# Optimization experiments

Measured on AMD Instinct MI355X. Metric: run time of the kernel, lower is better.

The kernel has to match this reference:

```python
import jax, jax.numpy as jnp
import numpy as np

B, M = 32768, 200
NUM_LAYERS, OW, OH = 22, 11, 11
CNN_CH, HIDDEN = 128, 512
ACTION_NVEC = (9, 10)


def setup_inputs() -> dict:
    key = jax.random.key(0)
    ks = jax.random.split(key, 16)
    s = 0.02
    inp = {
        "observations": jax.random.randint(ks[0], (B, M, 3), 0, 256, dtype=jnp.int32),
        "max_vec": jnp.ones((NUM_LAYERS,), dtype=jnp.float32),
        "w_conv1": jax.random.normal(ks[1], (CNN_CH, NUM_LAYERS, 5, 5), jnp.float32) * s,
        "b_conv1": jnp.zeros((CNN_CH,), jnp.float32),
        "w_conv2": jax.random.normal(ks[2], (CNN_CH, CNN_CH, 3, 3), jnp.float32) * s,
        "b_conv2": jnp.zeros((CNN_CH,), jnp.float32),
        "w_fc": jax.random.normal(ks[3], (CNN_CH, HIDDEN // 2), jnp.float32) * s,
        "b_fc": jnp.zeros((HIDDEN // 2,), jnp.float32),
        "w_self": jax.random.normal(ks[4], (NUM_LAYERS, HIDDEN // 2), jnp.float32) * s,
        "b_self": jnp.zeros((HIDDEN // 2,), jnp.float32),
        "w_actor0": jax.random.normal(ks[5], (HIDDEN, ACTION_NVEC[0]), jnp.float32) * 0.01,
        "b_actor0": jnp.zeros((ACTION_NVEC[0],), jnp.float32),
        "w_actor1": jax.random.normal(ks[6], (HIDDEN, ACTION_NVEC[1]), jnp.float32) * 0.01,
        "b_actor1": jnp.zeros((ACTION_NVEC[1],), jnp.float32),
        "w_value": jax.random.normal(ks[7], (HIDDEN, 1), jnp.float32) * s,
        "b_value": jnp.zeros((1,), jnp.float32),
    }
    return inp


def _conv(x, w, b, stride):
    y = jax.lax.conv_general_dilated(
        x, w, window_strides=(stride, stride), padding="VALID",
        dimension_numbers=("NCHW", "OIHW", "NCHW"))
    return y + b[None, :, None, None]


def _encode(observations, max_vec, w_conv1, b_conv1, w_conv2, b_conv2,
            w_fc, b_fc, w_self, b_self):
    # torch: token_observations[token_observations == 255] = 0
    obs = jnp.where(observations == 255, 0, observations)
    coords = obs[..., 0]                       # [B, M]
    x_idx = (coords >> 4) & 15
    y_idx = coords & 15
    atr_idx = obs[..., 1]
    atr_val = obs[..., 2].astype(jnp.float32)
    # coords_byte != 255 is always True after the 255->0 rewrite above
    valid = (x_idx < OW) & (y_idx < OH) & (atr_idx < NUM_LAYERS)
    b_idx = jnp.broadcast_to(jnp.arange(obs.shape[0])[:, None], coords.shape)
    # route invalid tokens to a dummy batch slot B, then drop it
    b_idx = jnp.where(valid, b_idx, obs.shape[0])
    a_idx = jnp.where(valid, atr_idx, 0)
    xs = jnp.where(valid, x_idx, 0)
    ys = jnp.where(valid, y_idx, 0)
    box = jnp.zeros((obs.shape[0] + 1, NUM_LAYERS, OW, OH), jnp.float32)
    box = box.at[b_idx, a_idx, xs, ys].set(atr_val)[: obs.shape[0]]
    features = box / max_vec[None, :, None, None]
    self_feat = jax.nn.relu(features[:, :, 5, 5] @ w_self + b_self)   # [B, 256]
    h = jax.nn.relu(_conv(features, w_conv1, b_conv1, 3))             # [B,128,3,3]
    h = jax.nn.relu(_conv(h, w_conv2, b_conv2, 1))                    # [B,128,1,1]
    h = h.reshape(h.shape[0], -1)                                     # [B,128]
    cnn_feat = jax.nn.relu(h @ w_fc + b_fc)                           # [B,256]
    return jnp.concatenate([self_feat, cnn_feat], axis=1)             # [B,512]


def reference(observations, max_vec, w_conv1, b_conv1, w_conv2, b_conv2,
              w_fc, b_fc, w_self, b_self, w_actor0, b_actor0,
              w_actor1, b_actor1, w_value, b_value):
    hidden = _encode(observations, max_vec, w_conv1, b_conv1, w_conv2, b_conv2,
                     w_fc, b_fc, w_self, b_self)
    logits0 = hidden @ w_actor0 + b_actor0
    logits1 = hidden @ w_actor1 + b_actor1
    value = hidden @ w_value + b_value
    return (logits0, logits1, value, hidden)
```

## Files before the change

kernel.cpp:

```cpp
#include <hip/hip_runtime.h>
#include <hip/hip_bf16.h>

typedef unsigned int uint;
typedef unsigned short ushort;
typedef unsigned long long ull;
typedef __attribute__((ext_vector_type(8))) short short8;
typedef __attribute__((ext_vector_type(4))) float float4_;

#define B_TOT 32768
#define NL    22
#define HID0  ((long)B_TOT * 20)

#define W2F_OFF  0
#define WFCF_OFF 294912
#define WHF_OFF  360448
#define W1P_OFF  393216
#define H1_OFF   534272

__device__ __forceinline__ ushort f2bf(float v) {
  uint x = __float_as_uint(v);
  x += 0x7fffu + ((x >> 16) & 1u);
  return (ushort)(x >> 16);
}
__device__ __forceinline__ uint cvtpk(float lo, float hi) {
  uint r;
  asm volatile("v_cvt_pk_bf16_f32 %0, %1, %2" : "=v"(r) : "v"(lo), "v"(hi));
  return r;
}
struct u3 { uint x, y, z; };

extern "C" __global__ __launch_bounds__(256)
void k_prep(const float* __restrict__ wc1, const float* __restrict__ wc2,
            const float* __restrict__ wfc,
            const float* __restrict__ wa0, const float* __restrict__ wa1,
            const float* __restrict__ wv,
            ushort* __restrict__ w2f, ushort* __restrict__ wfcf,
            ushort* __restrict__ whf, uint* __restrict__ w1p)
{
  int i = blockIdx.x * 256 + threadIdx.x;
  if (i < 18432) {
    int l = i & 63, cg = (i >> 6) & 7, ks = i >> 9;
    int col = cg * 16 + (l & 15), kb = ks * 32 + (l >> 4) * 8;
    ushort t[8];
    #pragma unroll
    for (int j = 0; j < 8; ++j) t[j] = f2bf(wc2[col * 1152 + kb + j]);
    uint4 o = { (uint)t[0]|((uint)t[1]<<16), (uint)t[2]|((uint)t[3]<<16),
                (uint)t[4]|((uint)t[5]<<16), (uint)t[6]|((uint)t[7]<<16) };
    ((uint4*)w2f)[i] = o;
  } else if (i < 22528) {
    int i2 = i - 18432;
    int l = i2 & 63, cg = (i2 >> 6) & 15, ks = i2 >> 10;
    int col = cg * 16 + (l & 15), kb = ks * 32 + (l >> 4) * 8;
    ushort t[8];
    #pragma unroll
    for (int j = 0; j < 8; ++j) t[j] = f2bf(wfc[(kb + j) * 256 + col]);
    uint4 o = { (uint)t[0]|((uint)t[1]<<16), (uint)t[2]|((uint)t[3]<<16),
                (uint)t[4]|((uint)t[5]<<16), (uint)t[6]|((uint)t[7]<<16) };
    ((uint4*)wfcf)[i2] = o;
  } else if (i < 24576) {
    int i2 = i - 22528;
    int l = i2 & 63, cg = (i2 >> 6) & 1, ks = i2 >> 7;
    int col = cg * 16 + (l & 15), kb = ks * 32 + (l >> 4) * 8;
    ushort t[8];
    #pragma unroll
    for (int j = 0; j < 8; ++j) {
      int k = kb + j;
      float v = (col < 9)  ? wa0[k*9 + col]
              : (col < 19) ? wa1[k*10 + (col - 9)]
              : (col == 19) ? wv[k] : 0.f;
      t[j] = f2bf(v);
    }
    uint4 o = { (uint)t[0]|((uint)t[1]<<16), (uint)t[2]|((uint)t[3]<<16),
                (uint)t[4]|((uint)t[5]<<16), (uint)t[6]|((uint)t[7]<<16) };
    ((uint4*)whf)[i2] = o;
  } else if (i < 24576 + 35264) {
    int j = i - 24576;
    int l = j & 63, r = j >> 6;
    uint val = 0u;
    if (r < 550) {
      ushort lo_ = f2bf(wc1[(2*l)     * 550 + r]);
      ushort hi_ = f2bf(wc1[(2*l + 1) * 550 + r]);
      val = (uint)lo_ | ((uint)hi_ << 16);
    }
    w1p[j] = val;
  }
}

#define PROC_CONV(tk, acc0, acc1)                                          \
  {                                                                        \
    const int a = (int)((tk) >> 16), x = (int)(((tk) >> 12) & 15u),        \
              y = (int)(((tk) >> 8) & 15u);                                \
    const float rmv = __int_as_float(                                      \
        __builtin_amdgcn_readlane(__float_as_int(rm_own), a));             \
    const float fv = (float)((tk) & 255u) * rmv;                           \
    const int wbase = a * 25;                                              \
    _Pragma("unroll")                                                      \
    for (int ox = 0; ox < 3; ++ox) {                                       \
      int kx = x - 3 * ox;                                                 \
      if ((unsigned)kx > 4u) continue;              \
      _Pragma("unroll")                                                    \
      for (int oy = 0; oy < 3; ++oy) {                                     \
        int ky = y - 3 * oy;                                               \
        if ((unsigned)ky > 4u) continue;                                   \
        uint wu = w1p[(wbase + kx * 5 + ky) * 64 + lane];                  \
        acc0[ox*3+oy] = fmaf(fv, __uint_as_float(wu << 16),                \
                             acc0[ox*3+oy]);                               \
        acc1[ox*3+oy] = fmaf(fv, __uint_as_float(wu & 0xffff0000u),        \
                             acc1[ox*3+oy]);                               \
      }                                                                    \
    }                                                                      \
  }

extern "C" __global__ __launch_bounds__(256)
void k_encode(const int* __restrict__ obs, const float* __restrict__ maxvec,
              const uint* __restrict__ w1p, const float* __restrict__ bc1,
              const float* __restrict__ wself, const float* __restrict__ bself,
              float* __restrict__ out, ushort* __restrict__ h1g)
{
  __shared__ uint klist[8][64];

  const int tid = threadIdx.x, lane = tid & 63, w = tid >> 6;
  const long bA = (long)blockIdx.x * 8 + w * 2;
  const long bB = bA + 1;

  float rm_own = (lane < NL) ? (1.0f / maxvec[lane]) : 0.f;

  const uint* obA = (const uint*)obs + bA * 600;
  const uint* obB = (const uint*)obs + bB * 600;
  uint* klA = klist[w * 2 + 0];
  uint* klB = klist[w * 2 + 1];

  int cntA = 0, cntB = 0;
  #pragma unroll
  for (int r = 0; r < 4; ++r) {
    int m = r * 64 + lane;
    bool vA = false, vB = false; uint pkA = 0, pkB = 0;
    if (m < 200) {
      u3 tA = *(const u3*)(obA + m * 3);
      u3 tB = *(const u3*)(obB + m * 3);
      uint cA = tA.x, aA = tA.y, vvA = tA.z;
      uint cB = tB.x, aB = tB.y, vvB = tB.z;
      cA = (cA == 255u) ? 0u : cA;  aA = (aA == 255u) ? 0u : aA;  vvA = (vvA == 255u) ? 0u : vvA;
      cB = (cB == 255u) ? 0u : cB;  aB = (aB == 255u) ? 0u : aB;  vvB = (vvB == 255u) ? 0u : vvB;
      uint xA = (cA >> 4) & 15u, yA = cA & 15u;
      uint xB = (cB >> 4) & 15u, yB = cB & 15u;
      vA = (xA < 11u) && (yA < 11u) && (aA < NL);
      vB = (xB < 11u) && (yB < 11u) && (aB < NL);
      pkA = (aA << 16) | (xA << 12) | (yA << 8) | vvA;
      pkB = (aB << 16) | (xB << 12) | (yB << 8) | vvB;
    }
    ull balA = __ballot(vA);
    if (vA) {
      int pos = cntA + __popcll(balA & ((1ull << lane) - 1ull));
      if (pos < 64) klA[pos] = pkA;
    }
    cntA += __popcll(balA);
    ull balB = __ballot(vB);
    if (vB) {
      int pos = cntB + __popcll(balB & ((1ull << lane) - 1ull));
      if (pos < 64) klB[pos] = pkB;
    }
    cntB += __popcll(balB);
  }
  if (cntA > 64) cntA = 64;
  if (cntB > 64) cntB = 64;

  uint uA = (lane < cntA) ? klA[lane] : 0xffffffffu;
  uint uB = (lane < cntB) ? klB[lane] : 0xffffffffu;
  uint cellA = uA >> 8, cellB = uB >> 8;
  bool aliveA = (lane < cntA), aliveB = (lane < cntB);
  const int dmax = (cntA > cntB) ? cntA : cntB;
  for (int d = 1; d < dmax; ++d) {
    uint oA = __shfl_down(cellA, d);
    uint oB = __shfl_down(cellB, d);
    aliveA = aliveA && !((lane + d < cntA) && (oA == cellA));
    aliveB = aliveB && !((lane + d < cntB) && (oB == cellB));
  }
  const ull balA2 = __ballot(aliveA);
  const ull balB2 = __ballot(aliveB);

  float2 saA = {0.f,0.f}, sbA = {0.f,0.f}, saB = {0.f,0.f}, sbB = {0.f,0.f};
  {
    ull b55 = __ballot(aliveA && (((uA >> 12) & 15u) == 5u) && (((uA >> 8) & 15u) == 5u));
    while (b55) {
      int idx = __builtin_ctzll(b55); b55 &= b55 - 1ull;
      uint tk = (uint)__builtin_amdgcn_readlane((int)uA, idx);
      int a = tk >> 16;
      float rmv = __int_as_float(__builtin_amdgcn_readlane(__float_as_int(rm_own), a));
      float fv = (float)(tk & 255u) * rmv;
      const float2* ws2 = (const float2*)(wself + a * 256);
      float2 w0 = ws2[lane], w1 = ws2[64 + lane];
      saA.x = fmaf(fv, w0.x, saA.x);  saA.y = fmaf(fv, w0.y, saA.y);
      sbA.x = fmaf(fv, w1.x, sbA.x);  sbA.y = fmaf(fv, w1.y, sbA.y);
    }
    b55 = __ballot(aliveB && (((uB >> 12) & 15u) == 5u) && (((uB >> 8) & 15u) == 5u));
    while (b55) {
      int idx = __builtin_ctzll(b55); b55 &= b55 - 1ull;
      uint tk = (uint)__builtin_amdgcn_readlane((int)uB, idx);
      int a = tk >> 16;
      float rmv = __int_as_float(__builtin_amdgcn_readlane(__float_as_int(rm_own), a));
      float fv = (float)(tk & 255u) * rmv;
      const float2* ws2 = (const float2*)(wself + a * 256);
      float2 w0 = ws2[lane], w1 = ws2[64 + lane];
      saB.x = fmaf(fv, w0.x, saB.x);  saB.y = fmaf(fv, w0.y, saB.y);
      sbB.x = fmaf(fv, w1.x, sbB.x);  sbB.y = fmaf(fv, w1.y, sbB.y);
    }
  }

  float aA0[9] = {0,0,0,0,0,0,0,0,0}, aA1[9] = {0,0,0,0,0,0,0,0,0};
  float aB0[9] = {0,0,0,0,0,0,0,0,0}, aB1[9] = {0,0,0,0,0,0,0,0,0};
  ull mA = balA2, mB = balB2;
  while (mA | mB) {
    if (mA) {
      int idx = __builtin_ctzll(mA); mA &= mA - 1ull;
      const uint tk = (uint)__builtin_amdgcn_readlane((int)uA, idx);
      PROC_CONV(tk, aA0, aA1);
    }
    if (mB) {
      int idx = __builtin_ctzll(mB); mB &= mB - 1ull;
      const uint tk = (uint)__builtin_amdgcn_readlane((int)uB, idx);
      PROC_CONV(tk, aB0, aB1);
    }
  }

  const float2* bs2 = (const float2*)bself;
  const float2 bsp0 = bs2[lane], bsp1 = bs2[64 + lane];
  const float2 bc = ((const float2*)bc1)[lane];

  {
    float2 o0 = { fmaxf(saA.x + bsp0.x, 0.f), fmaxf(saA.y + bsp0.y, 0.f) };
    float2 o1 = { fmaxf(sbA.x + bsp1.x, 0.f), fmaxf(sbA.y + bsp1.y, 0.f) };
    float2* out2 = (float2*)(out + HID0 + bA * 512);
    out2[lane] = o0;  out2[64 + lane] = o1;
    uint wds[9];
    wds[0] = cvtpk(fmaxf(aA0[0]+bc.x,0.f), fmaxf(aA0[1]+bc.x,0.f));
    wds[1] = cvtpk(fmaxf(aA0[2]+bc.x,0.f), fmaxf(aA0[3]+bc.x,0.f));
    wds[2] = cvtpk(fmaxf(aA0[4]+bc.x,0.f), fmaxf(aA0[5]+bc.x,0.f));
    wds[3] = cvtpk(fmaxf(aA0[6]+bc.x,0.f), fmaxf(aA0[7]+bc.x,0.f));
    wds[4] = cvtpk(fmaxf(aA0[8]+bc.x,0.f), fmaxf(aA1[0]+bc.y,0.f));
    wds[5] = cvtpk(fmaxf(aA1[1]+bc.y,0.f), fmaxf(aA1[2]+bc.y,0.f));
    wds[6] = cvtpk(fmaxf(aA1[3]+bc.y,0.f), fmaxf(aA1[4]+bc.y,0.f));
    wds[7] = cvtpk(fmaxf(aA1[5]+bc.y,0.f), fmaxf(aA1[6]+bc.y,0.f));
    wds[8] = cvtpk(fmaxf(aA1[7]+bc.y,0.f), fmaxf(aA1[8]+bc.y,0.f));
    uint* dst = (uint*)h1g + bA * 576 + 9 * lane;
    #pragma unroll
    for (int j = 0; j < 9; ++j) dst[j] = wds[j];
  }
  {
    float2 o0 = { fmaxf(saB.x + bsp0.x, 0.f), fmaxf(saB.y + bsp0.y, 0.f) };
    float2 o1 = { fmaxf(sbB.x + bsp1.x, 0.f), fmaxf(sbB.y + bsp1.y, 0.f) };
    float2* out2 = (float2*)(out + HID0 + bB * 512);
    out2[lane] = o0;  out2[64 + lane] = o1;
    uint wds[9];
    wds[0] = cvtpk(fmaxf(aB0[0]+bc.x,0.f), fmaxf(aB0[1]+bc.x,0.f));
    wds[1] = cvtpk(fmaxf(aB0[2]+bc.x,0.f), fmaxf(aB0[3]+bc.x,0.f));
    wds[2] = cvtpk(fmaxf(aB0[4]+bc.x,0.f), fmaxf(aB0[5]+bc.x,0.f));
    wds[3] = cvtpk(fmaxf(aB0[6]+bc.x,0.f), fmaxf(aB0[7]+bc.x,0.f));
    wds[4] = cvtpk(fmaxf(aB0[8]+bc.x,0.f), fmaxf(aB1[0]+bc.y,0.f));
    wds[5] = cvtpk(fmaxf(aB1[1]+bc.y,0.f), fmaxf(aB1[2]+bc.y,0.f));
    wds[6] = cvtpk(fmaxf(aB1[3]+bc.y,0.f), fmaxf(aB1[4]+bc.y,0.f));
    wds[7] = cvtpk(fmaxf(aB1[5]+bc.y,0.f), fmaxf(aB1[6]+bc.y,0.f));
    wds[8] = cvtpk(fmaxf(aB1[7]+bc.y,0.f), fmaxf(aB1[8]+bc.y,0.f));
    uint* dst = (uint*)h1g + bB * 576 + 9 * lane;
    #pragma unroll
    for (int j = 0; j < 9; ++j) dst[j] = wds[j];
  }
}

extern "C" __global__ __launch_bounds__(256)
void k_mlp(const ushort* __restrict__ h1g, const ushort* __restrict__ w2f,
           const float* __restrict__ bc2, const ushort* __restrict__ wfcf,
           const float* __restrict__ bfc, const ushort* __restrict__ whf,
           const float* __restrict__ ba0, const float* __restrict__ ba1,
           const float* __restrict__ bv, float* __restrict__ out)
{
  __shared__ short  Abuf[2][4][64][8];
  __shared__ ushort h2A[16][64][8];

  const int tid = threadIdx.x, lane = tid & 63, w = tid >> 6;
  const int lo = lane & 15, hi = lane >> 4;
  const int bb = blockIdx.x, b0 = bb * 64;

  const short8* w2fv  = (const short8*)w2f;
  const short8* wfcfv = (const short8*)wfcf;
  const uint4*  A4    = (const uint4*)h1g;
  const long    arow  = (long)(b0 + (tid >> 2)) * 144 + (tid & 3);

  float4_ acc[4][2];
  #pragma unroll
  for (int cgi = 0; cgi < 2; ++cgi) {
    float bv_ = bc2[(2*w + cgi)*16 + lo];
    float4_ t = {bv_, bv_, bv_, bv_};
    #pragma unroll
    for (int m = 0; m < 4; ++m) acc[m][cgi] = t;
  }

  uint4 rA = A4[arow];
  for (int t = 0; t < 36; ++t) {
    const int cur = t & 1;
    *(uint4*)&Abuf[cur][tid & 3][tid >> 2][0] = rA;
    if (t + 1 < 36) rA = A4[arow + (t + 1) * 4];
    __syncthreads();
    short8 af[4];
    #pragma unroll
    for (int m = 0; m < 4; ++m)
      af[m] = *(const short8*)&Abuf[cur][hi][m*16 + lo][0];
    #pragma unroll
    for (int cgi = 0; cgi < 2; ++cgi) {
      short8 bf = w2fv[(t*8 + 2*w + cgi)*64 + lane];
      #pragma unroll
      for (int m = 0; m < 4; ++m)
        acc[m][cgi] = __builtin_amdgcn_mfma_f32_16x16x32_bf16(af[m], bf, acc[m][cgi], 0, 0, 0);
    }
  }
  __syncthreads();

  #pragma unroll
  for (int cgi = 0; cgi < 2; ++cgi) {
    int col = (2*w + cgi)*16 + lo;
    #pragma unroll
    for (int m = 0; m < 4; ++m)
      #pragma unroll
      for (int q = 0; q < 4; ++q) {
        int R = m*16 + hi*4 + q;
        h2A[col >> 3][R][col & 7] = f2bf(fmaxf(acc[m][cgi][q], 0.f));
      }
  }
  __syncthreads();

  float4_ acc2[4][4];
  #pragma unroll
  for (int cgi = 0; cgi < 4; ++cgi) {
    float bv_ = bfc[(4*w + cgi)*16 + lo];
    float4_ t = {bv_, bv_, bv_, bv_};
    #pragma unroll
    for (int m = 0; m < 4; ++m) acc2[m][cgi] = t;
  }
  #pragma unroll
  for (int ks = 0; ks < 4; ++ks) {
    short8 af[4];
    #pragma unroll
    for (int m = 0; m < 4; ++m)
      af[m] = *(const short8*)&h2A[ks*4 + hi][m*16 + lo][0];
    #pragma unroll
    for (int cgi = 0; cgi < 4; ++cgi) {
      short8 bf = wfcfv[(ks*16 + 4*w + cgi)*64 + lane];
      #pragma unroll
      for (int m = 0; m < 4; ++m)
        acc2[m][cgi] = __builtin_amdgcn_mfma_f32_16x16x32_bf16(af[m], bf, acc2[m][cgi], 0, 0, 0);
    }
  }

  #pragma unroll
  for (int cgi = 0; cgi < 4; ++cgi) {
    int col = (4*w + cgi)*16 + lo;
    #pragma unroll
    for (int m = 0; m < 4; ++m)
      #pragma unroll
      for (int q = 0; q < 4; ++q) {
        int R = m*16 + hi*4 + q;
        out[HID0 + (long)(b0 + R)*512 + 256 + col] = fmaxf(acc2[m][cgi][q], 0.f);
      }
  }
  __syncthreads();

  const short8* whfv = (const short8*)whf;
  float4_ acc3[2];
  #pragma unroll
  for (int cg = 0; cg < 2; ++cg) {
    int col = cg*16 + lo;
    float bias = (col < 9) ? ba0[col] : (col < 19) ? ba1[col - 9]
               : (col == 19) ? bv[0] : 0.f;
    float4_ t = {bias, bias, bias, bias};
    acc3[cg] = t;
  }

  const float* hrow = out + HID0 + (long)(b0 + w*16 + lo) * 512;
  #pragma unroll
  for (int ks = 0; ks < 16; ++ks) {
    float4_ f0 = *(const float4_*)(hrow + ks*32 + hi*8);
    float4_ f1 = *(const float4_*)(hrow + ks*32 + hi*8 + 4);
    union { short8 s; ushort u[8]; } afu;
    afu.u[0] = f2bf(f0[0]); afu.u[1] = f2bf(f0[1]);
    afu.u[2] = f2bf(f0[2]); afu.u[3] = f2bf(f0[3]);
    afu.u[4] = f2bf(f1[0]); afu.u[5] = f2bf(f1[1]);
    afu.u[6] = f2bf(f1[2]); afu.u[7] = f2bf(f1[3]);
    #pragma unroll
    for (int cg = 0; cg < 2; ++cg) {
      short8 bf = whfv[(ks*2 + cg)*64 + lane];
      acc3[cg] = __builtin_amdgcn_mfma_f32_16x16x32_bf16(afu.s, bf, acc3[cg], 0, 0, 0);
    }
  }

  #pragma unroll
  for (int cg = 0; cg < 2; ++cg) {
    int col = cg*16 + lo;
    #pragma unroll
    for (int q = 0; q < 4; ++q) {
      long R = b0 + w*16 + hi*4 + q;
      float v = acc3[cg][q];
      if (col < 9)        out[R*9 + col] = v;
      else if (col < 19)  out[(long)B_TOT*9 + R*10 + (col - 9)] = v;
      else if (col == 19) out[(long)B_TOT*19 + R] = v;
    }
  }
}

extern "C" void kernel_launch(void* const* d_in, const int* in_sizes, int n_in,
                              void* d_out, int out_size, void* d_ws, size_t ws_size,
                              hipStream_t stream) {
  const int* obs      = (const int*)d_in[0];
  const float* maxvec = (const float*)d_in[1];
  const float* wc1    = (const float*)d_in[2];
  const float* bc1    = (const float*)d_in[3];
  const float* wc2    = (const float*)d_in[4];
  const float* bc2    = (const float*)d_in[5];
  const float* wfc    = (const float*)d_in[6];
  const float* bfc    = (const float*)d_in[7];
  const float* wself  = (const float*)d_in[8];
  const float* bself  = (const float*)d_in[9];
  const float* wa0    = (const float*)d_in[10];
  const float* ba0    = (const float*)d_in[11];
  const float* wa1    = (const float*)d_in[12];
  const float* ba1    = (const float*)d_in[13];
  const float* wv     = (const float*)d_in[14];
  const float* bv     = (const float*)d_in[15];
  float* out          = (float*)d_out;

  char* ws = (char*)d_ws;
  ushort* w2f  = (ushort*)(ws + W2F_OFF);
  ushort* wfcf = (ushort*)(ws + WFCF_OFF);
  ushort* whf  = (ushort*)(ws + WHF_OFF);
  uint*   w1p  = (uint*)(ws + W1P_OFF);
  ushort* h1g  = (ushort*)(ws + H1_OFF);

  k_prep  <<<dim3(234),      dim3(256), 0, stream>>>(wc1, wc2, wfc, wa0, wa1, wv,
                                                     w2f, wfcf, whf, w1p);
  k_encode<<<dim3(B_TOT/8),  dim3(256), 0, stream>>>(obs, maxvec, w1p, bc1,
                                                     wself, bself, out, h1g);
  k_mlp   <<<dim3(B_TOT/64), dim3(256), 0, stream>>>(h1g, w2f, bc2, wfcf, bfc,
                                                     whf, ba0, ba1, bv, out);
}
```

Before: 105.4 us.

## Batch four tokens per iteration in conv1 scatter loop with hoisted weight loads

Rewrites the token-driven conv1 accumulation loop to handle two tokens from each of the two batch rows per iteration. All weight loads for those tokens are issued before any FMAs, to expose memory-level parallelism on the serial readlane→load→fma chain. The affected output window is computed in closed form: with a stride-3, 5x5 kernel each token touches at most a 2x2 block of outputs, so four loads replace the predicated per-output loads. Exhausted masks yield a zero token that contributes nothing. The cost is more registers and some wasted work when the two rows' token counts differ or are odd.

Measured after the change: 131.8 us. 1.25x slower.

```diff
diff --git a/kernel.cpp b/kernel.cpp
--- a/kernel.cpp
+++ b/kernel.cpp
@@ -86,29 +86,49 @@
   }
 }
 
-#define PROC_CONV(tk, acc0, acc1)                                          \
+#define TB_DECODE(S, tk)                                                   \
+  const uint a_##S = (tk) >> 16, x_##S = ((tk) >> 12) & 15u,               \
+             y_##S = ((tk) >> 8) & 15u, val_##S = (tk) & 255u;             \
+  const float rmv_##S = __int_as_float(                                    \
+      __builtin_amdgcn_readlane(__float_as_int(rm_own), a_##S));           \
+  const float fv_##S = (float)val_##S * rmv_##S;                           \
+  const int oxl_##S = (x_##S >= 5u) ? ((int)x_##S - 2) / 3 : 0;            \
+  const int oyl_##S = (y_##S >= 5u) ? ((int)y_##S - 2) / 3 : 0;            \
+  const int oxh_##S = ((int)x_##S / 3 > 2) ? 2 : (int)x_##S / 3;           \
+  const int oyh_##S = ((int)y_##S / 3 > 2) ? 2 : (int)y_##S / 3;           \
+  const bool nx_##S = oxh_##S > oxl_##S, ny_##S = oyh_##S > oyl_##S;       \
+  const int w00_##S = (int)a_##S * 25 + ((int)x_##S - 3*oxl_##S) * 5       \
+                      + ((int)y_##S - 3*oyl_##S);                          \
+  const int w01_##S = ny_##S ? (w00_##S - 3)  : w00_##S;                   \
+  const int w10_##S = nx_##S ? (w00_##S - 15) : w00_##S;                   \
+  const int w11_##S = (nx_##S && ny_##S) ? (w00_##S - 18) : w00_##S;       \
+  const uint u00_##S = w1p[w00_##S * 64 + lane];                           \
+  const uint u01_##S = w1p[w01_##S * 64 + lane];                           \
+  const uint u10_##S = w1p[w10_##S * 64 + lane];                           \
+  const uint u11_##S = w1p[w11_##S * 64 + lane];
+
+#define TB_FMA(S, acc0, acc1)                                              \
+  _Pragma("unroll")                                                        \
+  for (int ox = 0; ox < 3; ++ox) {                                         \
+    if (ox < oxl_##S || ox > oxh_##S) continue;     \
+    _Pragma("unroll")                                                      \
+    for (int oy = 0; oy < 3; ++oy) {                                       \
+      if (oy < oyl_##S || oy > oyh_##S) continue;                          \
+      uint wu = (ox == oxl_##S) ? ((oy == oyl_##S) ? u00_##S : u01_##S)    \
+                                : ((oy == oyl_##S) ? u10_##S : u11_##S);   \
+      acc0[ox*3+oy] = fmaf(fv_##S, __uint_as_float(wu << 16),              \
+                           acc0[ox*3+oy]);                                 \
+      acc1[ox*3+oy] = fmaf(fv_##S, __uint_as_float(wu & 0xffff0000u),      \
+                           acc1[ox*3+oy]);                                 \
+    }                                                                      \
+  }
+
+#define NEXT_TOKEN(m, u, tk)                                               \
   {                                                                        \
-    const int a = (int)((tk) >> 16), x = (int)(((tk) >> 12) & 15u),        \
-              y = (int)(((tk) >> 8) & 15u);                                \
-    const float rmv = __int_as_float(                                      \
-        __builtin_amdgcn_readlane(__float_as_int(rm_own), a));             \
-    const float fv = (float)((tk) & 255u) * rmv;                           \
-    const int wbase = a * 25;                                              \
-    _Pragma("unroll")                                                      \
-    for (int ox = 0; ox < 3; ++ox) {                                       \
-      int kx = x - 3 * ox;                                                 \
-      if ((unsigned)kx > 4u) continue;              \
-      _Pragma("unroll")                                                    \
-      for (int oy = 0; oy < 3; ++oy) {                                     \
-        int ky = y - 3 * oy;                                               \
-        if ((unsigned)ky > 4u) continue;                                   \
-        uint wu = w1p[(wbase + kx * 5 + ky) * 64 + lane];                  \
-        acc0[ox*3+oy] = fmaf(fv, __uint_as_float(wu << 16),                \
-                             acc0[ox*3+oy]);                               \
-        acc1[ox*3+oy] = fmaf(fv, __uint_as_float(wu & 0xffff0000u),        \
-                             acc1[ox*3+oy]);                               \
-      }                                                                    \
-    }                                                                      \
+    int _i = __builtin_ctzll((m) | 0x8000000000000000ull);                 \
+    uint _t = (uint)__builtin_amdgcn_readlane((int)(u), _i);               \
+    (tk) = (m) ? _t : 0u;                                                  \
+    (m) &= (m) - 1ull;                                                     \
   }
 
 extern "C" __global__ __launch_bounds__(256)
@@ -210,17 +230,23 @@
   float aA0[9] = {0,0,0,0,0,0,0,0,0}, aA1[9] = {0,0,0,0,0,0,0,0,0};
   float aB0[9] = {0,0,0,0,0,0,0,0,0}, aB1[9] = {0,0,0,0,0,0,0,0,0};
   ull mA = balA2, mB = balB2;
-  while (mA | mB) {
-    if (mA) {
-      int idx = __builtin_ctzll(mA); mA &= mA - 1ull;
-      const uint tk = (uint)__builtin_amdgcn_readlane((int)uA, idx);
-      PROC_CONV(tk, aA0, aA1);
-    }
-    if (mB) {
-      int idx = __builtin_ctzll(mB); mB &= mB - 1ull;
-      const uint tk = (uint)__builtin_amdgcn_readlane((int)uB, idx);
-      PROC_CONV(tk, aB0, aB1);
-    }
+  int tmax;
+  { int pa = __popcll(mA), pb = __popcll(mB);
+    int mx = pa > pb ? pa : pb;  tmax = (mx + 1) >> 1; }
+  for (int t = 0; t < tmax; ++t) {
+    uint tkA0, tkA1, tkB0, tkB1;
+    NEXT_TOKEN(mA, uA, tkA0)
+    NEXT_TOKEN(mA, uA, tkA1)
+    NEXT_TOKEN(mB, uB, tkB0)
+    NEXT_TOKEN(mB, uB, tkB1)
+    TB_DECODE(A0, tkA0)
+    TB_DECODE(A1, tkA1)
+    TB_DECODE(B0, tkB0)
+    TB_DECODE(B1, tkB1)
+    TB_FMA(A0, aA0, aA1)
+    TB_FMA(A1, aA0, aA1)
+    TB_FMA(B0, aB0, aB1)
+    TB_FMA(B1, aB0, aB1)
   }
 
   const float2* bs2 = (const float2*)bself;
```
